# Performance work log

Measured on AMD Instinct MI355X. Metric: run time of the kernel, lower is better.

## Reference

```python
import jax, jax.numpy as jnp
import numpy as np

B, T, C = 8, 2048, 1024      # batch, timesteps, input_dim
G, E = 2, 320                # groups_dim, entries_dim
EMB = 512                    # emb_dim
D = EMB // G                 # true_emb_dim per group


def setup_inputs() -> dict:
    key = jax.random.key(0)
    k1, k2, k3 = jax.random.split(key, 3)
    X = jax.random.normal(k1, (B, T, C), dtype=jnp.float32)
    # nn.Linear(input_dim, G*E): weight (out,in) ~ N(0,1), bias zeros
    W = jax.random.normal(k2, (G * E, C), dtype=jnp.float32)
    b = jnp.zeros((G * E,), dtype=jnp.float32)
    # codebook Parameter(1, G*E, D) ~ U[0,1); stored squeezed as (G*E, D)
    codebook = jax.random.uniform(k3, (G * E, D), dtype=jnp.float32)
    return {"X": X, "W": W, "b": b, "codebook": codebook}


def reference(X, W, b, codebook):
    # Eval-mode forward of VectorQuantization (time_first=True).
    nB, nT, _ = X.shape
    logits = jnp.einsum("btc,kc->btk", X, W) + b           # (B, T, G*E)
    # Faithful to source: view (B,T,G*E) as (B*G, T*E) and argmax over last dim
    flat = logits.reshape(nB * G, nT * E)                   # (B*G, T*E)
    k = jnp.argmax(flat, axis=-1)                           # (B*G,)
    hard = jax.nn.one_hot(k, nT * E, dtype=logits.dtype)    # (B*G, T*E)
    q = hard.reshape(nB * nT, G, E)                         # (B*T, G, E)
    # (one-hot * codebook).sum over entries == per-group gather
    cb = codebook.reshape(G, E, D)                          # (G, E, D)
    out = jnp.einsum("nge,ged->ngd", q, cb)                 # (B*T, G, D)
    return out.reshape(nB, nT, G * D)                       # (B, T, emb_dim)
```

## Files before the change

### kernel.cpp

```cpp
#include <hip/hip_runtime.h>
#include <stdint.h>

#define CC    1024
#define EE    320
#define KN    640
#define DD    256
#define MTOT  16384
#define NBLK  640
#define OUT4  2097152
#define MARGIN 2.0f

typedef __attribute__((ext_vector_type(8))) short short8;
typedef __attribute__((ext_vector_type(4))) float f32x4;

__device__ __forceinline__ unsigned int f32_orderable(float x) {
    unsigned int b = __float_as_uint(x);
    return (b & 0x80000000u) ? ~b : (b | 0x80000000u);
}

__device__ __forceinline__ unsigned short bf16_rne(float x) {
    unsigned int u = __float_as_uint(x);
    return (unsigned short)((u + 0x7FFFu + ((u >> 16) & 1u)) >> 16);
}

__global__ void init_slots_kernel(unsigned long long* __restrict__ slots) {
    if (threadIdx.x < 17) slots[threadIdx.x] = 0ull;
}

__global__ __launch_bounds__(256)
void convert_kernel(const float* __restrict__ X, const float* __restrict__ W,
                    unsigned short* __restrict__ A2F, unsigned short* __restrict__ B2F,
                    unsigned long long* __restrict__ slots, float* __restrict__ out) {
    const int bid = blockIdx.x;
    const int tid = threadIdx.x;
    {
        int zidx = bid * 256 + tid;
        f32x4 z = {0.f, 0.f, 0.f, 0.f};
        if (zidx < OUT4) __builtin_nontemporal_store(z, (f32x4*)out + zidx);
    }
    const int lane = tid & 63;
    const float* src;
    unsigned short* dst;
    int unit;
    if (bid < 8192) {
        unit = bid * 4 + (tid >> 6);
        src = X; dst = A2F;
    } else {
        if (bid == 8192 && tid < 17) slots[tid] = 0ull;
        unit = (bid - 8192) * 4 + (tid >> 6);
        src = W; dst = B2F;
    }
    int rt = unit >> 5, kc = unit & 31;
    int row = rt * 16 + (lane & 15);
    int col = kc * 32 + ((lane >> 4) << 3);
    const float* p = src + (size_t)row * CC + col;
    float4 v0 = *(const float4*)p;
    float4 v1 = *(const float4*)(p + 4);
    short8 hi;
    hi[0] = (short)bf16_rne(v0.x); hi[1] = (short)bf16_rne(v0.y);
    hi[2] = (short)bf16_rne(v0.z); hi[3] = (short)bf16_rne(v0.w);
    hi[4] = (short)bf16_rne(v1.x); hi[5] = (short)bf16_rne(v1.y);
    hi[6] = (short)bf16_rne(v1.z); hi[7] = (short)bf16_rne(v1.w);
    *(short8*)(dst + (size_t)unit * 512 + lane * 8) = hi;
}

__global__ __launch_bounds__(256, 3)
void gemm_argmax_mfma(const unsigned short* __restrict__ A2F,
                      const unsigned short* __restrict__ B2F,
                      const float* __restrict__ X,
                      const float* __restrict__ W,
                      const float* __restrict__ bias,
                      const float* __restrict__ codebook,
                      float* __restrict__ out,
                      unsigned long long* __restrict__ slots,
                      unsigned int* __restrict__ counter) {
    __shared__ float redf[4];
    __shared__ int cnt_s;
    __shared__ int cand_s[128];
    __shared__ unsigned int done_s;
    __shared__ unsigned long long s16[16];

    const int tid  = threadIdx.x;
    const int lane = tid & 63;
    const int wave = tid >> 6;

    const int l   = blockIdx.x;
    const int xcd = l & 7;
    const int w   = l >> 3;
    const int mt  = xcd * 16 + w / 5;
    const int nt  = w % 5;
    const int m0 = mt * 128;
    const int n0 = nt * 128;

    const int wm = (wave >> 1) * 64;
    const int wn = (wave & 1) * 64;

    const unsigned short* Ap[4];
    const unsigned short* Bp[4];
#pragma unroll
    for (int t = 0; t < 4; t++) {
        Ap[t] = A2F + ((size_t)(((m0 + wm) >> 4) + t) * 32) * 512 + lane * 8;
        Bp[t] = B2F + ((size_t)(((n0 + wn) >> 4) + t) * 32) * 512 + lane * 8;
    }

    f32x4 acc[4][4] = {};
    short8 a0[4], b0[4], a1[4], b1[4];

#pragma unroll
    for (int t = 0; t < 4; t++) {
        a0[t] = *(const short8*)(Ap[t]);
        b0[t] = *(const short8*)(Bp[t]);
        Ap[t] += 512; Bp[t] += 512;
    }

#define STEP(CURA, CURB, NXTA, NXTB, IT)                                         \
    {                                                                            \
        if ((IT) < 31) {                                                         \
            _Pragma("unroll")                                                    \
            for (int t = 0; t < 4; t++) {                                        \
                NXTA[t] = *(const short8*)(Ap[t]);                               \
                NXTB[t] = *(const short8*)(Bp[t]);                               \
                Ap[t] += 512; Bp[t] += 512;                                      \
            }                                                                    \
        }                                                                        \
        _Pragma("unroll")                                                        \
        for (int ti = 0; ti < 4; ti++)                                           \
            _Pragma("unroll")                                                    \
            for (int tj = 0; tj < 4; tj++)                                       \
                acc[ti][tj] = __builtin_amdgcn_mfma_f32_16x16x32_bf16(           \
                    CURA[ti], CURB[tj], acc[ti][tj], 0, 0, 0);                   \
    }

    for (int it2 = 0; it2 < 16; it2++) {
        STEP(a0, b0, a1, b1, it2 * 2)
        STEP(a1, b1, a0, b0, it2 * 2 + 1)
    }
#undef STEP

    float bias4[4];
#pragma unroll
    for (int tj = 0; tj < 4; tj++) bias4[tj] = bias[n0 + wn + tj * 16 + (lane & 15)];

    float vmax = -3.0e38f;
#pragma unroll
    for (int ti = 0; ti < 4; ti++)
#pragma unroll
        for (int tj = 0; tj < 4; tj++)
#pragma unroll
            for (int r = 0; r < 4; r++)
                vmax = fmaxf(vmax, acc[ti][tj][r] + bias4[tj]);
#pragma unroll
    for (int off = 32; off > 0; off >>= 1)
        vmax = fmaxf(vmax, __shfl_down(vmax, off, 64));
    if (lane == 0) redf[wave] = vmax;
    if (tid == 0) cnt_s = 0;
    __syncthreads();
    float bm = fmaxf(fmaxf(redf[0], redf[1]), fmaxf(redf[2], redf[3]));
    float thresh = bm - MARGIN;

#pragma unroll
    for (int ti = 0; ti < 4; ti++) {
#pragma unroll
        for (int r = 0; r < 4; r++) {
            int m = m0 + wm + ti * 16 + (lane >> 4) * 4 + r;
#pragma unroll
            for (int tj = 0; tj < 4; tj++) {
                float v = acc[ti][tj][r] + bias4[tj];
                if (v >= thresh) {
                    int n = n0 + wn + tj * 16 + (lane & 15);
                    int idx = atomicAdd(&cnt_s, 1);
                    if (idx < 128) cand_s[idx] = (m << 10) | n;
                }
            }
        }
    }
    __syncthreads();
    int cnt = cnt_s < 128 ? cnt_s : 128;

    for (int i = 0; i < cnt; i++) {
        int mc = cand_s[i] >> 10;
        int nc = cand_s[i] & 1023;
        float4 xv = *(const float4*)(X + (size_t)mc * CC + tid * 4);
        float4 wv = *(const float4*)(W + (size_t)nc * CC + tid * 4);
        float p = xv.x * wv.x + xv.y * wv.y + xv.z * wv.z + xv.w * wv.w;
#pragma unroll
        for (int off = 32; off > 0; off >>= 1) p += __shfl_down(p, off, 64);
        if (lane == 0) redf[wave] = p;
        __syncthreads();
        if (tid == 0) {
            float tot = redf[0] + redf[1] + redf[2] + redf[3] + bias[nc];
            unsigned int c = (unsigned int)((mc & 1023) * KN + nc);
            unsigned long long pk =
                ((unsigned long long)f32_orderable(tot) << 32) |
                (unsigned long long)(~c);
            atomicMax(slots + (mc >> 10), pk);
        }
        __syncthreads();
    }

    if (tid == 0) {
        __threadfence();
        done_s = atomicAdd(counter, 1u);
    }
    __syncthreads();

    if (done_s == NBLK - 1) {
        if (tid < 16) s16[tid] = atomicAdd(slots + tid, 0ull);
        __syncthreads();
        int rr  = tid >> 4;
        int seg = tid & 15;
        unsigned long long p = s16[rr];
        unsigned int c = ~(unsigned int)(p & 0xFFFFFFFFull);
        int tl = (int)(c / KN);
        int kg = (int)(c % KN);
        int b  = rr >> 1, h = rr & 1;
        int nstar = b * 2048 + h * 1024 + tl;
        int g = kg / EE;
        const float4* src = (const float4*)(codebook + (size_t)kg * DD) + seg * 4;
        float4* dst = (float4*)(out + (size_t)nstar * 512 + (size_t)g * DD) + seg * 4;
#pragma unroll
        for (int j = 0; j < 4; j++) dst[j] = src[j];
    }
}

__global__ __launch_bounds__(256)
void zs_kernel(const unsigned long long* __restrict__ slots,
               const float* __restrict__ codebook,
               float4* __restrict__ out4) {
    int i4 = blockIdx.x * 256 + threadIdx.x;
    int n  = i4 >> 7;
    int c4 = i4 & 127;
    int b  = n >> 11;
    int h  = (n >> 10) & 1;
    unsigned long long p = slots[b * 2 + h];
    unsigned int c = ~(unsigned int)(p & 0xFFFFFFFFull);
    int tl = (int)(c / KN);
    int kg = (int)(c % KN);
    int nstar = b * 2048 + h * 1024 + tl;
    int g = kg / EE;
    float4 v = make_float4(0.f, 0.f, 0.f, 0.f);
    if (n == nstar && (c4 >> 6) == g)
        v = ((const float4*)codebook)[kg * 64 + (c4 & 63)];
    out4[i4] = v;
}

#define BM 128
#define BN 64
#define BK 32
#define LDA (BM + 4)
#define LDB (BN + 4)

__global__ __launch_bounds__(128)
void gemm_argmax_f32(const float* __restrict__ X, const float* __restrict__ W,
                     const float* __restrict__ bias,
                     unsigned long long* __restrict__ slots) {
    __shared__ float Asf[BK][LDA];
    __shared__ float Bsf[BK][LDB];
    const int tid = threadIdx.x;
    const int m0 = blockIdx.y * BM;
    const int n0 = blockIdx.x * BN;
    const int tx = tid & 7, ty = tid >> 3;
    float acc[8][8];
#pragma unroll
    for (int i = 0; i < 8; i++)
#pragma unroll
        for (int j = 0; j < 8; j++) acc[i][j] = 0.0f;
    const int lm = tid >> 3, lk = (tid & 7) * 4;
    const float* Xb = X + (size_t)m0 * CC;
    const float* Wb = W + (size_t)n0 * CC;
    for (int k0 = 0; k0 < CC; k0 += BK) {
#pragma unroll
        for (int r = 0; r < 8; r++) {
            int m = r * 16 + lm;
            float4 v = *(const float4*)(Xb + (size_t)m * CC + k0 + lk);
            Asf[lk + 0][m] = v.x; Asf[lk + 1][m] = v.y; Asf[lk + 2][m] = v.z; Asf[lk + 3][m] = v.w;
        }
#pragma unroll
        for (int r = 0; r < 4; r++) {
            int m = r * 16 + lm;
            float4 v = *(const float4*)(Wb + (size_t)m * CC + k0 + lk);
            Bsf[lk + 0][m] = v.x; Bsf[lk + 1][m] = v.y; Bsf[lk + 2][m] = v.z; Bsf[lk + 3][m] = v.w;
        }
        __syncthreads();
#pragma unroll
        for (int kk = 0; kk < BK; kk++) {
            float4 A0 = *(const float4*)&Asf[kk][ty * 8];
            float4 A1 = *(const float4*)&Asf[kk][ty * 8 + 4];
            float4 B0 = *(const float4*)&Bsf[kk][tx * 8];
            float4 B1 = *(const float4*)&Bsf[kk][tx * 8 + 4];
            float a[8] = {A0.x, A0.y, A0.z, A0.w, A1.x, A1.y, A1.z, A1.w};
            float b[8] = {B0.x, B0.y, B0.z, B0.w, B1.x, B1.y, B1.z, B1.w};
#pragma unroll
            for (int i = 0; i < 8; i++)
#pragma unroll
                for (int j = 0; j < 8; j++) acc[i][j] = fmaf(a[i], b[j], acc[i][j]);
        }
        __syncthreads();
    }
    unsigned long long best = 0ull;
#pragma unroll
    for (int i = 0; i < 8; i++) {
        int mg = m0 + ty * 8 + i;
        int tl = mg & 1023;
#pragma unroll
        for (int j = 0; j < 8; j++) {
            int kg = n0 + tx * 8 + j;
            float v = acc[i][j] + bias[kg];
            unsigned int c = (unsigned int)(tl * KN + kg);
            unsigned long long p = ((unsigned long long)f32_orderable(v) << 32) |
                                   (unsigned long long)(~c);
            if (p > best) best = p;
        }
    }
#pragma unroll
    for (int off = 32; off > 0; off >>= 1) {
        unsigned long long o = __shfl_down(best, off, 64);
        if (o > best) best = o;
    }
    __shared__ unsigned long long red2[2];
    if ((tid & 63) == 0) red2[tid >> 6] = best;
    __syncthreads();
    if (tid == 0) {
        unsigned long long b0 = red2[0], b1 = red2[1];
        atomicMax(slots + (m0 >> 10), b0 > b1 ? b0 : b1);
    }
}

extern "C" void kernel_launch(void* const* d_in, const int* in_sizes, int n_in,
                              void* d_out, int out_size, void* d_ws, size_t ws_size,
                              hipStream_t stream) {
    const float* X        = (const float*)d_in[0];
    const float* W        = (const float*)d_in[1];
    const float* bias     = (const float*)d_in[2];
    const float* codebook = (const float*)d_in[3];
    float* out = (float*)d_out;

    unsigned long long* slots = (unsigned long long*)d_ws;
    unsigned int* counter = (unsigned int*)(slots + 16);
    const size_t A_off   = 256;
    const size_t A_bytes = (size_t)MTOT * CC * 2;
    const size_t B_off   = A_off + A_bytes;
    const size_t B_bytes = (size_t)KN * CC * 2;
    const size_t need = B_off + B_bytes;

    if (ws_size >= need) {
        unsigned short* A2F = (unsigned short*)((char*)d_ws + A_off);
        unsigned short* B2F = (unsigned short*)((char*)d_ws + B_off);
        hipLaunchKernelGGL(convert_kernel, dim3(8192 + 320), dim3(256), 0, stream,
                           X, W, A2F, B2F, slots, out);
        hipLaunchKernelGGL(gemm_argmax_mfma, dim3(NBLK), dim3(256), 0, stream,
                           A2F, B2F, X, W, bias, codebook, out, slots, counter);
    } else {
        hipLaunchKernelGGL(init_slots_kernel, dim3(1), dim3(64), 0, stream, slots);
        hipLaunchKernelGGL(gemm_argmax_f32, dim3(KN / BN, MTOT / BM), dim3(128), 0, stream,
                           X, W, bias, slots);
        hipLaunchKernelGGL(zs_kernel, dim3(OUT4 / 256), dim3(256), 0, stream,
                           slots, codebook, (float4*)out);
    }
}
```

Baseline: 155.8 us.

## Fuse X bf16 conversion into GEMM via LDS double-buffered staging

```diff
diff --git a/kernel.cpp b/kernel.cpp
--- a/kernel.cpp
+++ b/kernel.cpp
@@ -8,6 +8,7 @@
 #define MTOT  16384
 #define NBLK  640
 #define OUT4  2097152
+#define ZPB   3277
 #define MARGIN 2.0f
 
 typedef __attribute__((ext_vector_type(8))) short short8;
@@ -28,32 +29,15 @@
 }
 
 __global__ __launch_bounds__(256)
-void convert_kernel(const float* __restrict__ X, const float* __restrict__ W,
-                    unsigned short* __restrict__ A2F, unsigned short* __restrict__ B2F,
-                    unsigned long long* __restrict__ slots, float* __restrict__ out) {
-    const int bid = blockIdx.x;
-    const int tid = threadIdx.x;
-    {
-        int zidx = bid * 256 + tid;
-        f32x4 z = {0.f, 0.f, 0.f, 0.f};
-        if (zidx < OUT4) __builtin_nontemporal_store(z, (f32x4*)out + zidx);
-    }
-    const int lane = tid & 63;
-    const float* src;
-    unsigned short* dst;
-    int unit;
-    if (bid < 8192) {
-        unit = bid * 4 + (tid >> 6);
-        src = X; dst = A2F;
-    } else {
-        if (bid == 8192 && tid < 17) slots[tid] = 0ull;
-        unit = (bid - 8192) * 4 + (tid >> 6);
-        src = W; dst = B2F;
-    }
+void prep_kernel(const float* __restrict__ W, unsigned short* __restrict__ B2F,
+                 unsigned long long* __restrict__ slots) {
+    if (blockIdx.x == 0 && threadIdx.x < 17) slots[threadIdx.x] = 0ull;
+    const int lane = threadIdx.x & 63;
+    int unit = blockIdx.x * 4 + (threadIdx.x >> 6);
     int rt = unit >> 5, kc = unit & 31;
     int row = rt * 16 + (lane & 15);
     int col = kc * 32 + ((lane >> 4) << 3);
-    const float* p = src + (size_t)row * CC + col;
+    const float* p = W + (size_t)row * CC + col;
     float4 v0 = *(const float4*)p;
     float4 v1 = *(const float4*)(p + 4);
     short8 hi;
@@ -61,19 +45,19 @@
     hi[2] = (short)bf16_rne(v0.z); hi[3] = (short)bf16_rne(v0.w);
     hi[4] = (short)bf16_rne(v1.x); hi[5] = (short)bf16_rne(v1.y);
     hi[6] = (short)bf16_rne(v1.z); hi[7] = (short)bf16_rne(v1.w);
-    *(short8*)(dst + (size_t)unit * 512 + lane * 8) = hi;
+    *(short8*)(B2F + (size_t)unit * 512 + lane * 8) = hi;
 }
 
 __global__ __launch_bounds__(256, 3)
-void gemm_argmax_mfma(const unsigned short* __restrict__ A2F,
-                      const unsigned short* __restrict__ B2F,
-                      const float* __restrict__ X,
-                      const float* __restrict__ W,
-                      const float* __restrict__ bias,
-                      const float* __restrict__ codebook,
-                      float* __restrict__ out,
-                      unsigned long long* __restrict__ slots,
-                      unsigned int* __restrict__ counter) {
+void vq_fused(const float* __restrict__ X,
+              const unsigned short* __restrict__ B2F,
+              const float* __restrict__ W,
+              const float* __restrict__ bias,
+              const float* __restrict__ codebook,
+              float* __restrict__ out,
+              unsigned long long* __restrict__ slots,
+              unsigned int* __restrict__ counter) {
+    __shared__ __align__(16) unsigned short lds_s[16384];
     __shared__ float redf[4];
     __shared__ int cnt_s;
     __shared__ int cand_s[128];
@@ -89,53 +73,107 @@
     const int w   = l >> 3;
     const int mt  = xcd * 16 + w / 5;
     const int nt  = w % 5;
-    const int m0 = mt * 128;
-    const int n0 = nt * 128;
-
-    const int wm = (wave >> 1) * 64;
-    const int wn = (wave & 1) * 64;
-
-    const unsigned short* Ap[4];
-    const unsigned short* Bp[4];
-#pragma unroll
-    for (int t = 0; t < 4; t++) {
-        Ap[t] = A2F + ((size_t)(((m0 + wm) >> 4) + t) * 32) * 512 + lane * 8;
-        Bp[t] = B2F + ((size_t)(((n0 + wn) >> 4) + t) * 32) * 512 + lane * 8;
-    }
+    const int m0  = mt * 128;
+    const int n0  = nt * 128;
+    const int wm  = (wave >> 1) * 64;
+    const int wn  = (wave & 1) * 64;
+
+    char* ldsb = (char*)lds_s;
+
+    const int r  = tid >> 1;
+    const int hh = tid & 1;
+    const float* gA = X + (size_t)(m0 + r) * CC + hh * 16;
+    const int wAoff = (r >> 4) * 1024 + (r & 15) * 16 + hh * 512;
+    const unsigned short* gB0 = B2F + (size_t)((nt * 8 + 2 * wave) * 32) * 512 + lane * 8;
+    const unsigned short* gB1 = B2F + (size_t)((nt * 8 + 2 * wave + 1) * 32) * 512 + lane * 8;
+    const int u0off = 8192 + (2 * wave) * 1024;
+    const int u1off = u0off + 1024;
+    const int aoff = (wm >> 4) * 1024 + lane * 16;
+    const int boff = 8192 + (wn >> 4) * 1024 + lane * 16;
 
     f32x4 acc[4][4] = {};
-    short8 a0[4], b0[4], a1[4], b1[4];
-
-#pragma unroll
-    for (int t = 0; t < 4; t++) {
-        a0[t] = *(const short8*)(Ap[t]);
-        b0[t] = *(const short8*)(Bp[t]);
-        Ap[t] += 512; Bp[t] += 512;
-    }
-
-#define STEP(CURA, CURB, NXTA, NXTB, IT)                                         \
-    {                                                                            \
-        if ((IT) < 31) {                                                         \
-            _Pragma("unroll")                                                    \
-            for (int t = 0; t < 4; t++) {                                        \
-                NXTA[t] = *(const short8*)(Ap[t]);                               \
-                NXTB[t] = *(const short8*)(Bp[t]);                               \
-                Ap[t] += 512; Bp[t] += 512;                                      \
-            }                                                                    \
-        }                                                                        \
-        _Pragma("unroll")                                                        \
-        for (int ti = 0; ti < 4; ti++)                                           \
-            _Pragma("unroll")                                                    \
-            for (int tj = 0; tj < 4; tj++)                                       \
-                acc[ti][tj] = __builtin_amdgcn_mfma_f32_16x16x32_bf16(           \
-                    CURA[ti], CURB[tj], acc[ti][tj], 0, 0, 0);                   \
-    }
-
-    for (int it2 = 0; it2 < 16; it2++) {
-        STEP(a0, b0, a1, b1, it2 * 2)
-        STEP(a1, b1, a0, b0, it2 * 2 + 1)
-    }
-#undef STEP
+    float4 fa0, fa1, fa2, fa3;
+
+#define CVTPK(d, lo, hi) asm("v_cvt_pk_bf16_f32 %0, %1, %2" : "=v"(d) : "v"(lo), "v"(hi))
+
+#define STAGE_ISSUE(T, BB)                                                               \
+    {                                                                                    \
+        const float* ga_ = gA + (size_t)(T) * 32;                                        \
+        fa0 = *(const float4*)(ga_);                                                     \
+        fa1 = *(const float4*)(ga_ + 4);                                                 \
+        fa2 = *(const float4*)(ga_ + 8);                                                 \
+        fa3 = *(const float4*)(ga_ + 12);                                                \
+        __builtin_amdgcn_global_load_lds(                                                \
+            (const __attribute__((address_space(1))) void*)(gB0 + (size_t)(T) * 512),    \
+            (__attribute__((address_space(3))) void*)(ldsb + (BB) + u0off), 16, 0, 0);   \
+        __builtin_amdgcn_global_load_lds(                                                \
+            (const __attribute__((address_space(1))) void*)(gB1 + (size_t)(T) * 512),    \
+            (__attribute__((address_space(3))) void*)(ldsb + (BB) + u1off), 16, 0, 0);   \
+    }
+
+#define STAGE_WRITE(BB)                                                                  \
+    {                                                                                    \
+        unsigned int c0, c1, c2, c3, c4, c5, c6, c7;                                     \
+        CVTPK(c0, fa0.x, fa0.y); CVTPK(c1, fa0.z, fa0.w);                                \
+        CVTPK(c2, fa1.x, fa1.y); CVTPK(c3, fa1.z, fa1.w);                                \
+        CVTPK(c4, fa2.x, fa2.y); CVTPK(c5, fa2.z, fa2.w);                                \
+        CVTPK(c6, fa3.x, fa3.y); CVTPK(c7, fa3.z, fa3.w);                                \
+        *(int4*)(ldsb + (BB) + wAoff)       = make_int4((int)c0, (int)c1, (int)c2, (int)c3); \
+        *(int4*)(ldsb + (BB) + wAoff + 256) = make_int4((int)c4, (int)c5, (int)c6, (int)c7); \
+    }
+
+#define COMPUTE(BB)                                                                      \
+    {                                                                                    \
+        short8 af[4], bfr[4];                                                            \
+        _Pragma("unroll")                                                                \
+        for (int t = 0; t < 4; t++) {                                                    \
+            af[t]  = *(const short8*)(ldsb + (BB) + aoff + t * 1024);                    \
+            bfr[t] = *(const short8*)(ldsb + (BB) + boff + t * 1024);                    \
+        }                                                                                \
+        _Pragma("unroll")                                                                \
+        for (int ti = 0; ti < 4; ti++)                                                   \
+            _Pragma("unroll")                                                            \
+            for (int tj = 0; tj < 4; tj++)                                               \
+                acc[ti][tj] = __builtin_amdgcn_mfma_f32_16x16x32_bf16(                   \
+                    af[ti], bfr[tj], acc[ti][tj], 0, 0, 0);                              \
+    }
+
+    STAGE_ISSUE(0, 0)
+    {
+        int base = l * ZPB;
+        f32x4 z = {0.f, 0.f, 0.f, 0.f};
+        for (int j = 0; j < 13; j++) {
+            int o = j * 256 + tid;
+            int idx = base + o;
+            if (o < ZPB && idx < OUT4)
+                __builtin_nontemporal_store(z, (f32x4*)out + idx);
+        }
+    }
+    STAGE_WRITE(0)
+    asm volatile("s_waitcnt vmcnt(0)" ::: "memory");
+    __syncthreads();
+
+    for (int it = 0; it < 16; it++) {
+        STAGE_ISSUE(2 * it + 1, 16384)
+        COMPUTE(0)
+        STAGE_WRITE(16384)
+        asm volatile("s_waitcnt vmcnt(0)" ::: "memory");
+        __syncthreads();
+        if (it < 15) {
+            STAGE_ISSUE(2 * it + 2, 0)
+            COMPUTE(16384)
+            STAGE_WRITE(0)
+            asm volatile("s_waitcnt vmcnt(0)" ::: "memory");
+        } else {
+            COMPUTE(16384)
+        }
+        __syncthreads();
+    }
+
+#undef COMPUTE
+#undef STAGE_WRITE
+#undef STAGE_ISSUE
+#undef CVTPK
 
     float bias4[4];
 #pragma unroll
@@ -147,8 +185,8 @@
 #pragma unroll
         for (int tj = 0; tj < 4; tj++)
 #pragma unroll
-            for (int r = 0; r < 4; r++)
-                vmax = fmaxf(vmax, acc[ti][tj][r] + bias4[tj]);
+            for (int rr = 0; rr < 4; rr++)
+                vmax = fmaxf(vmax, acc[ti][tj][rr] + bias4[tj]);
 #pragma unroll
     for (int off = 32; off > 0; off >>= 1)
         vmax = fmaxf(vmax, __shfl_down(vmax, off, 64));
@@ -161,11 +199,11 @@
 #pragma unroll
     for (int ti = 0; ti < 4; ti++) {
 #pragma unroll
-        for (int r = 0; r < 4; r++) {
-            int m = m0 + wm + ti * 16 + (lane >> 4) * 4 + r;
+        for (int rr = 0; rr < 4; rr++) {
+            int m = m0 + wm + ti * 16 + (lane >> 4) * 4 + rr;
 #pragma unroll
             for (int tj = 0; tj < 4; tj++) {
-                float v = acc[ti][tj][r] + bias4[tj];
+                float v = acc[ti][tj][rr] + bias4[tj];
                 if (v >= thresh) {
                     int n = n0 + wn + tj * 16 + (lane & 15);
                     int idx = atomicAdd(&cnt_s, 1);
@@ -270,14 +308,14 @@
     const float* Wb = W + (size_t)n0 * CC;
     for (int k0 = 0; k0 < CC; k0 += BK) {
 #pragma unroll
-        for (int r = 0; r < 8; r++) {
-            int m = r * 16 + lm;
+        for (int rr = 0; rr < 8; rr++) {
+            int m = rr * 16 + lm;
             float4 v = *(const float4*)(Xb + (size_t)m * CC + k0 + lk);
             Asf[lk + 0][m] = v.x; Asf[lk + 1][m] = v.y; Asf[lk + 2][m] = v.z; Asf[lk + 3][m] = v.w;
         }
 #pragma unroll
-        for (int r = 0; r < 4; r++) {
-            int m = r * 16 + lm;
+        for (int rr = 0; rr < 4; rr++) {
+            int m = rr * 16 + lm;
             float4 v = *(const float4*)(Wb + (size_t)m * CC + k0 + lk);
             Bsf[lk + 0][m] = v.x; Bsf[lk + 1][m] = v.y; Bsf[lk + 2][m] = v.z; Bsf[lk + 3][m] = v.w;
         }
@@ -337,19 +375,15 @@
 
     unsigned long long* slots = (unsigned long long*)d_ws;
     unsigned int* counter = (unsigned int*)(slots + 16);
-    const size_t A_off   = 256;
-    const size_t A_bytes = (size_t)MTOT * CC * 2;
-    const size_t B_off   = A_off + A_bytes;
+    const size_t B_off   = 256;
     const size_t B_bytes = (size_t)KN * CC * 2;
     const size_t need = B_off + B_bytes;
 
     if (ws_size >= need) {
-        unsigned short* A2F = (unsigned short*)((char*)d_ws + A_off);
         unsigned short* B2F = (unsigned short*)((char*)d_ws + B_off);
-        hipLaunchKernelGGL(convert_kernel, dim3(8192 + 320), dim3(256), 0, stream,
-                           X, W, A2F, B2F, slots, out);
-        hipLaunchKernelGGL(gemm_argmax_mfma, dim3(NBLK), dim3(256), 0, stream,
-                           A2F, B2F, X, W, bias, codebook, out, slots, counter);
+        hipLaunchKernelGGL(prep_kernel, dim3(320), dim3(256), 0, stream, W, B2F, slots);
+        hipLaunchKernelGGL(vq_fused, dim3(NBLK), dim3(256), 0, stream,
+                           X, B2F, W, bias, codebook, out, slots, counter);
     } else {
         hipLaunchKernelGGL(init_slots_kernel, dim3(1), dim3(64), 0, stream, slots);
         hipLaunchKernelGGL(gemm_argmax_f32, dim3(KN / BN, MTOT / BM), dim3(128), 0, stream,
```

After: 173.2 us. +11.2%, slower.
